# Kernel optimization log

Measured on AMD Instinct MI355X. Metric: run time of the kernel, lower is better.

Reference implementation:

```python
import jax, jax.numpy as jnp
import numpy as np

ALPHA = 0.2          # LeakyReLU negative slope
NEG_INF = -9e15      # mask value from the torch code
B, N, F, E, H, S, T, L = 32, 128, 78, 12, 256, 20, 13, 3


def setup_inputs() -> dict:
    key = jax.random.key(0)
    ks = jax.random.split(key, 20)
    sc = 0.05  # param scale
    inp = {
        "node_features": jax.random.normal(ks[0], (B, N, F), jnp.float32),
        "edge_features": jax.random.normal(ks[1], (B, N, N, E), jnp.float32),
        "adj_matrix": jax.random.randint(ks[2], (B, N, N), 0, 2).astype(jnp.int32),
        "scaffold_features": jax.random.normal(ks[3], (B, S), jnp.float32),
        # node projection (Linear F->H, with bias)
        "W_node": jax.random.normal(ks[4], (F, H), jnp.float32) * sc,
        "b_node": jnp.zeros((H,), jnp.float32),
        # stacked GAT layer params: W (H->H, no bias), a (2H->1, no bias)
        "gat_W": jax.random.normal(ks[5], (L, H, H), jnp.float32) * sc,
        "gat_a": jax.random.normal(ks[6], (L, 2 * H), jnp.float32) * sc,
        # scaffold projection (S->H)
        "W_sc": jax.random.normal(ks[7], (S, H), jnp.float32) * sc,
        "b_sc": jnp.zeros((H,), jnp.float32),
        # graph_pooling MLP: H -> H/2 -> H/4 (shared for graph + scaffold paths)
        "gp_w1": jax.random.normal(ks[8], (H, H // 2), jnp.float32) * sc,
        "gp_b1": jnp.zeros((H // 2,), jnp.float32),
        "gp_w2": jax.random.normal(ks[9], (H // 2, H // 4), jnp.float32) * sc,
        "gp_b2": jnp.zeros((H // 4,), jnp.float32),
        # output MLP: (H/4 + H/4) -> H/2 -> T
        "out_w1": jax.random.normal(ks[10], (H // 2, H // 2), jnp.float32) * sc,
        "out_b1": jnp.zeros((H // 2,), jnp.float32),
        "out_w2": jax.random.normal(ks[11], (H // 2, T), jnp.float32) * sc,
        "out_b2": jnp.zeros((T,), jnp.float32),
    }
    return inp


def _gat_stack(x, adj_matrix, gat_W, gat_a):
    # x: (B,N,H); adj: (B,N,N) int
    mask = adj_matrix > 0
    n_layers, _, h_dim = gat_W.shape
    for l in range(n_layers):
        h = jnp.einsum("bnf,fh->bnh", x, gat_W[l])      # (B,N,H)
        a1, a2 = gat_a[l, :h_dim], gat_a[l, h_dim:]
        # a . [h_i ; h_j] == h_i.a1 + h_j.a2 (exact decomposition of the
        # O(N^2, 2H) concat in the torch code)
        s1 = h @ a1                                       # (B,N)
        s2 = h @ a2                                       # (B,N)
        e = jax.nn.leaky_relu(s1[:, :, None] + s2[:, None, :], ALPHA)
        att = jnp.where(mask, e, NEG_INF)                 # (B,N,N)
        att = jax.nn.softmax(att, axis=-1)
        h_prime = jnp.einsum("bij,bjh->bih", att, h)
        x = jax.nn.relu(h_prime)                          # relu after layer (dropout = identity, eval)
    return x


def _pool(z, gp_w1, gp_b1, gp_w2, gp_b2):
    z = jax.nn.relu(z @ gp_w1 + gp_b1)
    return jax.nn.relu(z @ gp_w2 + gp_b2)


def reference(node_features, edge_features, adj_matrix, scaffold_features,
              W_node, b_node, gat_W, gat_a, W_sc, b_sc,
              gp_w1, gp_b1, gp_w2, gp_b2, out_w1, out_b1, out_w2, out_b2):
    # edge_features is accepted but unused in the original forward
    x = node_features @ W_node + b_node                  # (B,N,H)
    x = _gat_stack(x, adj_matrix, gat_W, gat_a)
    graph = x.mean(axis=1)                               # (B,H)
    g = _pool(graph, gp_w1, gp_b1, gp_w2, gp_b2)         # (B,H/4)
    s = _pool(scaffold_features @ W_sc + b_sc, gp_w1, gp_b1, gp_w2, gp_b2)
    c = jnp.concatenate([g, s], axis=-1)                 # (B,H/2)
    hdn = jax.nn.relu(c @ out_w1 + out_b1)
    return hdn @ out_w2 + out_b2                         # (B,T)
```

## Files before the change

### kernel.cpp

```cpp
#include <hip/hip_runtime.h>
#include <hip/hip_bf16.h>

#define NEG_INF -9.0e15f

using u16 = unsigned short;

__device__ __forceinline__ float b2f(__hip_bfloat16 v) { return __bfloat162float(v); }
__device__ __forceinline__ float ldv(const float* p, int i) { return p[i]; }
__device__ __forceinline__ float ldv(const __hip_bfloat16* p, int i) { return __bfloat162float(p[i]); }
__device__ __forceinline__ float bu2f(u16 u) { return __uint_as_float(((unsigned)u) << 16); }

__device__ __forceinline__ void unpack8u(uint4 r, float* f) {
    f[0]=__uint_as_float(r.x<<16); f[1]=__uint_as_float(r.x&0xffff0000u);
    f[2]=__uint_as_float(r.y<<16); f[3]=__uint_as_float(r.y&0xffff0000u);
    f[4]=__uint_as_float(r.z<<16); f[5]=__uint_as_float(r.z&0xffff0000u);
    f[6]=__uint_as_float(r.w<<16); f[7]=__uint_as_float(r.w&0xffff0000u);
}

__device__ __forceinline__ void async16(const void* g, void* l) {
    __builtin_amdgcn_global_load_lds(
        (__attribute__((address_space(1))) void*)(g),
        (__attribute__((address_space(3))) void*)(l), 16, 0, 0);
}

__device__ __forceinline__ int sniff(const void* wnode) {
    const u16* w = (const u16*)wnode;
    int lane = threadIdx.x & 63;
    u16 u = w[2 * lane];
    int e = (u >> 7) & 0xFF;
    unsigned long long m = __ballot(e >= 100 && e <= 140);
    return __popcll(m) >= 48;
}

__global__ __launch_bounds__(128) void k_gat(
    const float* __restrict__ x, const void* __restrict__ gat_W,
    const void* __restrict__ gat_a, int layer,
    const void* __restrict__ nf, const void* __restrict__ Wn_raw,
    const void* __restrict__ bn, int first,
    float* __restrict__ h, float* __restrict__ s1, float* __restrict__ s2) {
    __shared__ __align__(16) char smem[8192 + 32768 + 2560];
    float* xsT = (float*)smem;
    char*  wb  = smem + 8192;
    float* nfs = (float*)(smem + 8192 + 32768);

    const int t = threadIdx.x, bx = blockIdx.x;
    const int row0 = bx * 8;
    const int rg = t >> 5, cg = t & 31, c0 = 8 * cg;
    const int isbf = sniff(Wn_raw);
    float acc0[8], acc1[8];

    if (isbf) {
        const u16* Wl = (const u16*)gat_W + (size_t)layer * 65536;
        {
            const char* g = (const char*)Wl;
            #pragma unroll
            for (int i = 0; i < 8; ++i)
                async16(g + i * 2048 + t * 16, wb + i * 2048 + t * 16);
        }
        if (first) {
            const u16* nfu = (const u16*)nf;
            for (int i = t; i < 624; i += 128) {
                int r = i / 78, k = i - r * 78;
                nfs[r * 80 + k] = bu2f(nfu[(row0 + r) * 78 + k]);
            }
            __syncthreads();
            const u16* Wnl = (const u16*)Wn_raw;
            float b8[8];
            unpack8u(*(const uint4*)((const u16*)bn + c0), b8);
            #pragma unroll
            for (int j = 0; j < 8; ++j) { acc0[j] = b8[j]; acc1[j] = b8[j]; }
            #pragma unroll 2
            for (int k = 0; k < 78; ++k) {
                float w8[8];
                unpack8u(*(const uint4*)(Wnl + k * 256 + c0), w8);
                float x0 = nfs[(2 * rg) * 80 + k], x1 = nfs[(2 * rg + 1) * 80 + k];
                #pragma unroll
                for (int j = 0; j < 8; ++j) {
                    acc0[j] += x0 * w8[j];
                    acc1[j] += x1 * w8[j];
                }
            }
            #pragma unroll
            for (int j = 0; j < 8; ++j) {
                xsT[(c0 + j) * 8 + 2 * rg]     = acc0[j];
                xsT[(c0 + j) * 8 + 2 * rg + 1] = acc1[j];
            }
            __syncthreads();
        } else {
            int row = t >> 4, kb = (t & 15) * 16;
            const float4* xp = (const float4*)(x + (size_t)(row0 + row) * 256 + kb);
            #pragma unroll
            for (int q = 0; q < 4; ++q) {
                float4 f = xp[q];
                xsT[(kb + 4 * q + 0) * 8 + row] = f.x;
                xsT[(kb + 4 * q + 1) * 8 + row] = f.y;
                xsT[(kb + 4 * q + 2) * 8 + row] = f.z;
                xsT[(kb + 4 * q + 3) * 8 + row] = f.w;
            }
            __syncthreads();
        }
        #pragma unroll
        for (int j = 0; j < 8; ++j) { acc0[j] = 0.f; acc1[j] = 0.f; }
        for (int c = 0; c < 8; ++c) {
            if (c < 7) {
                const char* g = (const char*)Wl + (c + 1) * 16384;
                char* lb = wb + ((c + 1) & 1) * 16384;
                #pragma unroll
                for (int i = 0; i < 8; ++i)
                    async16(g + i * 2048 + t * 16, lb + i * 2048 + t * 16);
            }
            const u16* wc = (const u16*)(wb + (c & 1) * 16384);
            const float* xk = xsT + (c * 32) * 8 + 2 * rg;
            #pragma unroll 4
            for (int kk = 0; kk < 32; ++kk) {
                float w8[8];
                unpack8u(*(const uint4*)(wc + kk * 256 + c0), w8);
                float2 xv = *(const float2*)(xk + kk * 8);
                #pragma unroll
                for (int j = 0; j < 8; ++j) {
                    acc0[j] += xv.x * w8[j];
                    acc1[j] += xv.y * w8[j];
                }
            }
            __syncthreads();
        }
        const u16* ga = (const u16*)gat_a + (size_t)layer * 512;
        float a1v[8], a2v[8];
        unpack8u(*(const uint4*)(ga + c0), a1v);
        unpack8u(*(const uint4*)(ga + 256 + c0), a2v);
        float d10 = 0.f, d20 = 0.f, d11 = 0.f, d21 = 0.f;
        #pragma unroll
        for (int j = 0; j < 8; ++j) {
            d10 += acc0[j] * a1v[j]; d20 += acc0[j] * a2v[j];
            d11 += acc1[j] * a1v[j]; d21 += acc1[j] * a2v[j];
        }
        #pragma unroll
        for (int off = 1; off < 32; off <<= 1) {
            d10 += __shfl_xor(d10, off, 64); d20 += __shfl_xor(d20, off, 64);
            d11 += __shfl_xor(d11, off, 64); d21 += __shfl_xor(d21, off, 64);
        }
        if (cg == 0) {
            s1[row0 + 2 * rg] = d10;     s2[row0 + 2 * rg] = d20;
            s1[row0 + 2 * rg + 1] = d11; s2[row0 + 2 * rg + 1] = d21;
        }
        *(float4*)&h[(size_t)(row0 + 2 * rg) * 256 + c0]         = (float4){acc0[0], acc0[1], acc0[2], acc0[3]};
        *(float4*)&h[(size_t)(row0 + 2 * rg) * 256 + c0 + 4]     = (float4){acc0[4], acc0[5], acc0[6], acc0[7]};
        *(float4*)&h[(size_t)(row0 + 2 * rg + 1) * 256 + c0]     = (float4){acc1[0], acc1[1], acc1[2], acc1[3]};
        *(float4*)&h[(size_t)(row0 + 2 * rg + 1) * 256 + c0 + 4] = (float4){acc1[4], acc1[5], acc1[6], acc1[7]};
    } else {
        float* xs = (float*)smem;
        const float* Wlf = (const float*)gat_W + (size_t)layer * 65536;
        const float* gaf = (const float*)gat_a + (size_t)layer * 512;
        if (first) {
            const float* nff = (const float*)nf;
            for (int i = t; i < 624; i += 128) {
                int r = i / 78, k = i - r * 78;
                nfs[r * 80 + k] = nff[(row0 + r) * 78 + k];
            }
            __syncthreads();
            const float* Wnf = (const float*)Wn_raw;
            const float* bnf = (const float*)bn;
            #pragma unroll
            for (int j = 0; j < 8; ++j) { acc0[j] = bnf[c0 + j]; acc1[j] = acc0[j]; }
            for (int k = 0; k < 78; ++k) {
                float4 w0 = *(const float4*)(Wnf + k * 256 + c0);
                float4 w1 = *(const float4*)(Wnf + k * 256 + c0 + 4);
                float wf[8] = {w0.x, w0.y, w0.z, w0.w, w1.x, w1.y, w1.z, w1.w};
                float x0 = nfs[(2 * rg) * 80 + k], x1 = nfs[(2 * rg + 1) * 80 + k];
                #pragma unroll
                for (int j = 0; j < 8; ++j) { acc0[j] += x0 * wf[j]; acc1[j] += x1 * wf[j]; }
            }
            __syncthreads();
            #pragma unroll
            for (int j = 0; j < 8; ++j) {
                xs[(2 * rg) * 256 + c0 + j]     = acc0[j];
                xs[(2 * rg + 1) * 256 + c0 + j] = acc1[j];
            }
            __syncthreads();
        } else {
            int row = t >> 4, kb = (t & 15) * 16;
            #pragma unroll
            for (int q = 0; q < 4; ++q)
                ((float4*)(xs + row * 256 + kb))[q] =
                    ((const float4*)(x + (size_t)(row0 + row) * 256 + kb))[q];
            __syncthreads();
        }
        #pragma unroll
        for (int j = 0; j < 8; ++j) { acc0[j] = 0.f; acc1[j] = 0.f; }
        #pragma unroll 4
        for (int k = 0; k < 256; ++k) {
            float4 w0 = *(const float4*)(Wlf + k * 256 + c0);
            float4 w1 = *(const float4*)(Wlf + k * 256 + c0 + 4);
            float wf[8] = {w0.x, w0.y, w0.z, w0.w, w1.x, w1.y, w1.z, w1.w};
            float x0 = xs[(2 * rg) * 256 + k], x1 = xs[(2 * rg + 1) * 256 + k];
            #pragma unroll
            for (int j = 0; j < 8; ++j) { acc0[j] += x0 * wf[j]; acc1[j] += x1 * wf[j]; }
        }
        float d10 = 0.f, d20 = 0.f, d11 = 0.f, d21 = 0.f;
        #pragma unroll
        for (int j = 0; j < 8; ++j) {
            float a1v = gaf[c0 + j], a2v = gaf[256 + c0 + j];
            d10 += acc0[j] * a1v; d20 += acc0[j] * a2v;
            d11 += acc1[j] * a1v; d21 += acc1[j] * a2v;
        }
        #pragma unroll
        for (int off = 1; off < 32; off <<= 1) {
            d10 += __shfl_xor(d10, off, 64); d20 += __shfl_xor(d20, off, 64);
            d11 += __shfl_xor(d11, off, 64); d21 += __shfl_xor(d21, off, 64);
        }
        if (cg == 0) {
            s1[row0 + 2 * rg] = d10;     s2[row0 + 2 * rg] = d20;
            s1[row0 + 2 * rg + 1] = d11; s2[row0 + 2 * rg + 1] = d21;
        }
        *(float4*)&h[(size_t)(row0 + 2 * rg) * 256 + c0]         = (float4){acc0[0], acc0[1], acc0[2], acc0[3]};
        *(float4*)&h[(size_t)(row0 + 2 * rg) * 256 + c0 + 4]     = (float4){acc0[4], acc0[5], acc0[6], acc0[7]};
        *(float4*)&h[(size_t)(row0 + 2 * rg + 1) * 256 + c0]     = (float4){acc1[0], acc1[1], acc1[2], acc1[3]};
        *(float4*)&h[(size_t)(row0 + 2 * rg + 1) * 256 + c0 + 4] = (float4){acc1[4], acc1[5], acc1[6], acc1[7]};
    }
}

__global__ __launch_bounds__(256) void k_attn(
    const float* __restrict__ h, const float* __restrict__ s1,
    const float* __restrict__ s2, const int* __restrict__ adj,
    float* __restrict__ x, float* __restrict__ gpart, int do_pool) {
    __shared__ float att_t[128][10];
    __shared__ __align__(16) float hbuf[2][32 * 256];
    __shared__ float pool_red[4][256];
    int blk = blockIdx.x, b = blk >> 4, i0 = (blk & 15) << 3;
    int t = threadIdx.x, w = t >> 6, lane = t & 63;
    const char* hbytes = (const char*)(h + (size_t)b * 32768);
    const int ph = blk & 3;
    {
        char* lb = (char*)&hbuf[0][0];
        const char* g = hbytes + ph * 32768;
        #pragma unroll
        for (int i = 0; i < 8; ++i)
            async16(g + i * 4096 + t * 16, lb + i * 4096 + t * 16);
    }
    {
        int cc0 = lane, cc1 = lane + 64;
        int ir0 = i0 + 2 * w, ir1 = ir0 + 1;
        const int* a0 = adj + (size_t)(b * 128 + ir0) * 128;
        const int* a1 = adj + (size_t)(b * 128 + ir1) * 128;
        int m00 = a0[cc0], m01 = a0[cc1], m10 = a1[cc0], m11 = a1[cc1];
        float sv0 = s1[b * 128 + ir0], sv1 = s1[b * 128 + ir1];
        float t0 = s2[b * 128 + cc0],  t1 = s2[b * 128 + cc1];
        float e00 = sv0 + t0; e00 = (e00 >= 0.f) ? e00 : 0.2f * e00;
        float e01 = sv0 + t1; e01 = (e01 >= 0.f) ? e01 : 0.2f * e01;
        float e10 = sv1 + t0; e10 = (e10 >= 0.f) ? e10 : 0.2f * e10;
        float e11 = sv1 + t1; e11 = (e11 >= 0.f) ? e11 : 0.2f * e11;
        float v00 = (m00 > 0) ? e00 : NEG_INF;
        float v01 = (m01 > 0) ? e01 : NEG_INF;
        float v10 = (m10 > 0) ? e10 : NEG_INF;
        float v11 = (m11 > 0) ? e11 : NEG_INF;
        float mx0 = fmaxf(v00, v01), mx1 = fmaxf(v10, v11);
        #pragma unroll
        for (int off = 1; off < 64; off <<= 1) {
            mx0 = fmaxf(mx0, __shfl_xor(mx0, off, 64));
            mx1 = fmaxf(mx1, __shfl_xor(mx1, off, 64));
        }
        float p00 = __expf(v00 - mx0), p01 = __expf(v01 - mx0);
        float p10 = __expf(v10 - mx1), p11 = __expf(v11 - mx1);
        float s0 = p00 + p01, ss1 = p10 + p11;
        #pragma unroll
        for (int off = 1; off < 64; off <<= 1) {
            s0  += __shfl_xor(s0, off, 64);
            ss1 += __shfl_xor(ss1, off, 64);
        }
        float inv0 = 1.0f / s0, inv1 = 1.0f / ss1;
        att_t[cc0][2 * w]     = p00 * inv0;
        att_t[cc1][2 * w]     = p01 * inv0;
        att_t[cc0][2 * w + 1] = p10 * inv1;
        att_t[cc1][2 * w + 1] = p11 * inv1;
    }
    __syncthreads();
    int tx = t & 63, ty = t >> 6;
    float acc0[4] = {0.f, 0.f, 0.f, 0.f}, acc1[4] = {0.f, 0.f, 0.f, 0.f};
    for (int c = 0; c < 4; ++c) {
        if (c < 3) {
            char* lb = (char*)&hbuf[(c + 1) & 1][0];
            const char* g = hbytes + (((c + 1 + ph) & 3) * 32768);
            #pragma unroll
            for (int i = 0; i < 8; ++i)
                async16(g + i * 4096 + t * 16, lb + i * 4096 + t * 16);
        }
        const float* hc = &hbuf[c & 1][0];
        const int jb = ((c + ph) & 3) * 32;
        #pragma unroll 4
        for (int jj = 0; jj < 32; ++jj) {
            float4 hv = *(const float4*)&hc[jj * 256 + 4 * tx];
            float2 ap = *(const float2*)&att_t[jb + jj][2 * ty];
            acc0[0] += ap.x * hv.x; acc0[1] += ap.x * hv.y;
            acc0[2] += ap.x * hv.z; acc0[3] += ap.x * hv.w;
            acc1[0] += ap.y * hv.x; acc1[1] += ap.y * hv.y;
            acc1[2] += ap.y * hv.z; acc1[3] += ap.y * hv.w;
        }
        __syncthreads();
    }
    if (!do_pool) {
        float4 o0 = {fmaxf(acc0[0],0.f), fmaxf(acc0[1],0.f), fmaxf(acc0[2],0.f), fmaxf(acc0[3],0.f)};
        float4 o1 = {fmaxf(acc1[0],0.f), fmaxf(acc1[1],0.f), fmaxf(acc1[2],0.f), fmaxf(acc1[3],0.f)};
        *(float4*)&x[(size_t)(b * 128 + i0 + 2 * ty)     * 256 + 4 * tx] = o0;
        *(float4*)&x[(size_t)(b * 128 + i0 + 2 * ty + 1) * 256 + 4 * tx] = o1;
    } else {
        float4 pr = {(fmaxf(acc0[0],0.f) + fmaxf(acc1[0],0.f)) * (1.f/128.f),
                     (fmaxf(acc0[1],0.f) + fmaxf(acc1[1],0.f)) * (1.f/128.f),
                     (fmaxf(acc0[2],0.f) + fmaxf(acc1[2],0.f)) * (1.f/128.f),
                     (fmaxf(acc0[3],0.f) + fmaxf(acc1[3],0.f)) * (1.f/128.f)};
        *(float4*)&pool_red[ty][4 * tx] = pr;
        __syncthreads();
        if (t < 64) {
            float4 r0 = ((const float4*)&pool_red[0][0])[t];
            float4 r1 = ((const float4*)&pool_red[1][0])[t];
            float4 r2 = ((const float4*)&pool_red[2][0])[t];
            float4 r3 = ((const float4*)&pool_red[3][0])[t];
            float4 o = {r0.x+r1.x+r2.x+r3.x, r0.y+r1.y+r2.y+r3.y,
                        r0.z+r1.z+r2.z+r3.z, r0.w+r1.w+r2.w+r3.w};
            *(float4*)&gpart[((size_t)b * 16 + (blk & 15)) * 256 + 4 * t] = o;
        }
    }
}

template <typename T>
__device__ __forceinline__ void head_body(
    int b, int t, const float* __restrict__ gpart,
    const T* scaf, const T* W_sc, const T* b_sc,
    const T* gp_w1, const T* gp_b1, const T* gp_w2, const T* gp_b2,
    const T* out_w1, const T* out_b1, const T* out_w2, const T* out_b2,
    float* gin_s, float* sproj, float* scaf_s,
    float* red1, float* red2, float* z1g, float* z1s,
    float* cvec, float* hdn, float* outv) {
    float g = 0.f;
    #pragma unroll
    for (int gg = 0; gg < 16; ++gg) g += gpart[((size_t)b * 16 + gg) * 256 + t];
    gin_s[t] = g;
    if (t < 20) scaf_s[t] = ldv(scaf, b * 20 + t);
    __syncthreads();
    {
        float sa = ldv(b_sc, t);
        #pragma unroll
        for (int k = 0; k < 20; ++k) sa += scaf_s[k] * ldv(W_sc, k * 256 + t);
        sproj[t] = sa;
    }
    __syncthreads();
    {
        int j = t & 127, khalf = t >> 7;
        int k0 = khalf * 128;
        float a1 = 0.f, a2 = 0.f;
        #pragma unroll 16
        for (int kk = 0; kk < 128; ++kk) {
            int k = k0 + kk;
            float wv = ldv(gp_w1, k * 128 + j);
            a1 += gin_s[k] * wv;
            a2 += sproj[k] * wv;
        }
        red1[t] = a1; red2[t] = a2;
    }
    __syncthreads();
    if (t < 128) {
        float bb = ldv(gp_b1, t);
        z1g[t] = fmaxf(bb + red1[t] + red1[t + 128], 0.f);
        z1s[t] = fmaxf(bb + red2[t] + red2[t + 128], 0.f);
    }
    __syncthreads();
    {
        int j = t & 63, q = t >> 6;
        int k0 = q * 32;
        float a1 = 0.f, a2 = 0.f;
        #pragma unroll
        for (int kk = 0; kk < 32; ++kk) {
            int k = k0 + kk;
            float wv = ldv(gp_w2, k * 64 + j);
            a1 += z1g[k] * wv;
            a2 += z1s[k] * wv;
        }
        red1[t] = a1; red2[t] = a2;
    }
    __syncthreads();
    if (t < 64) {
        float bb = ldv(gp_b2, t);
        cvec[t]      = fmaxf(bb + red1[t] + red1[t + 64] + red1[t + 128] + red1[t + 192], 0.f);
        cvec[64 + t] = fmaxf(bb + red2[t] + red2[t + 64] + red2[t + 128] + red2[t + 192], 0.f);
    }
    __syncthreads();
    {
        int j = t & 127, khalf = t >> 7;
        int k0 = khalf * 64;
        float a = 0.f;
        #pragma unroll 16
        for (int kk = 0; kk < 64; ++kk) {
            int k = k0 + kk;
            a += cvec[k] * ldv(out_w1, k * 128 + j);
        }
        red1[t] = a;
    }
    __syncthreads();
    if (t < 128) hdn[t] = fmaxf(ldv(out_b1, t) + red1[t] + red1[t + 128], 0.f);
    __syncthreads();
    if (t < 13) {
        float a = ldv(out_b2, t);
        #pragma unroll 16
        for (int k = 0; k < 128; ++k) a += hdn[k] * ldv(out_w2, k * 13 + t);
        outv[t] = a;
    }
}

__global__ __launch_bounds__(256) void k_head(
    const float* __restrict__ gpart, const void* __restrict__ scaf,
    const void* __restrict__ W_sc, const void* __restrict__ b_sc,
    const void* __restrict__ gp_w1, const void* __restrict__ gp_b1,
    const void* __restrict__ gp_w2, const void* __restrict__ gp_b2,
    const void* __restrict__ out_w1, const void* __restrict__ out_b1,
    const void* __restrict__ out_w2, const void* __restrict__ out_b2,
    void* __restrict__ out, const void* __restrict__ Wn) {
    int isbf = sniff(Wn);
    int b = blockIdx.x;
    int t = threadIdx.x;
    __shared__ float gin_s[256], sproj[256], scaf_s[20];
    __shared__ float red1[256], red2[256];
    __shared__ float z1g[128], z1s[128], cvec[128], hdn[128], outv[13];
    if (isbf) {
        head_body<__hip_bfloat16>(b, t, gpart,
            (const __hip_bfloat16*)scaf, (const __hip_bfloat16*)W_sc, (const __hip_bfloat16*)b_sc,
            (const __hip_bfloat16*)gp_w1, (const __hip_bfloat16*)gp_b1,
            (const __hip_bfloat16*)gp_w2, (const __hip_bfloat16*)gp_b2,
            (const __hip_bfloat16*)out_w1, (const __hip_bfloat16*)out_b1,
            (const __hip_bfloat16*)out_w2, (const __hip_bfloat16*)out_b2,
            gin_s, sproj, scaf_s, red1, red2, z1g, z1s, cvec, hdn, outv);
    } else {
        head_body<float>(b, t, gpart,
            (const float*)scaf, (const float*)W_sc, (const float*)b_sc,
            (const float*)gp_w1, (const float*)gp_b1,
            (const float*)gp_w2, (const float*)gp_b2,
            (const float*)out_w1, (const float*)out_b1,
            (const float*)out_w2, (const float*)out_b2,
            gin_s, sproj, scaf_s, red1, red2, z1g, z1s, cvec, hdn, outv);
    }
    __syncthreads();
    if (t < 13) {
        if (isbf) ((__hip_bfloat16*)out)[b * 13 + t] = __float2bfloat16(outv[t]);
        else      ((float*)out)[b * 13 + t] = outv[t];
    }
}

extern "C" void kernel_launch(void* const* d_in, const int* in_sizes, int n_in,
                              void* d_out, int out_size, void* d_ws, size_t ws_size,
                              hipStream_t stream) {
    (void)in_sizes; (void)n_in; (void)out_size; (void)ws_size;
    const void* nf     = d_in[0];
    const int*  adj    = (const int*)d_in[2];
    const void* scaf   = d_in[3];
    const void* W_node = d_in[4];
    const void* b_node = d_in[5];
    const void* gat_W  = d_in[6];
    const void* gat_a  = d_in[7];
    const void* W_sc   = d_in[8];
    const void* b_sc   = d_in[9];
    const void* gp_w1  = d_in[10];
    const void* gp_b1  = d_in[11];
    const void* gp_w2  = d_in[12];
    const void* gp_b2  = d_in[13];
    const void* out_w1 = d_in[14];
    const void* out_b1 = d_in[15];
    const void* out_w2 = d_in[16];
    const void* out_b2 = d_in[17];

    float* ws    = (float*)d_ws;
    float* x     = ws;
    float* h     = ws + 1048576;
    float* s1    = ws + 2097152;
    float* s2    = s1 + 4096;
    float* gpart = s2 + 4096;

    for (int l = 0; l < 3; ++l) {
        k_gat<<<512, 128, 0, stream>>>(x, gat_W, gat_a, l,
                                       nf, W_node, b_node, (l == 0) ? 1 : 0,
                                       h, s1, s2);
        k_attn<<<512, 256, 0, stream>>>(h, s1, s2, adj, x, gpart, (l == 2) ? 1 : 0);
    }
    k_head<<<32, 256, 0, stream>>>(gpart, scaf, W_sc, b_sc, gp_w1, gp_b1, gp_w2, gp_b2,
                                   out_w1, out_b1, out_w2, out_b2, d_out, W_node);
}
```

Baseline: 229.0 us.

## Fuse attention aggregation with next layer's projection into a single kernel

Adds a kernel that computes the attention softmax and aggregation for one layer, applies ReLU, and immediately multiplies the resulting 8-row tile by the next layer's W to produce h, s1 and s2. This removes the round trip of x through global memory and cuts kernel launches from seven to five. The h tile is staged in smaller chunks with a per-block rotated start offset to spread load across memory. In exchange, each block streams the whole W matrix straight from global memory without LDS staging, and occupancy may drop because shared memory use is higher.

```diff
diff --git a/kernel.cpp b/kernel.cpp
--- a/kernel.cpp
+++ b/kernel.cpp
@@ -33,16 +33,14 @@
 }
 
 __global__ __launch_bounds__(128) void k_gat(
-    const float* __restrict__ x, const void* __restrict__ gat_W,
-    const void* __restrict__ gat_a, int layer,
+    const void* __restrict__ gat_W, const void* __restrict__ gat_a,
     const void* __restrict__ nf, const void* __restrict__ Wn_raw,
-    const void* __restrict__ bn, int first,
+    const void* __restrict__ bn,
     float* __restrict__ h, float* __restrict__ s1, float* __restrict__ s2) {
     __shared__ __align__(16) char smem[8192 + 32768 + 2560];
     float* xsT = (float*)smem;
     char*  wb  = smem + 8192;
     float* nfs = (float*)(smem + 8192 + 32768);
-
     const int t = threadIdx.x, bx = blockIdx.x;
     const int row0 = bx * 8;
     const int rg = t >> 5, cg = t & 31, c0 = 8 * cg;
@@ -50,55 +48,38 @@
     float acc0[8], acc1[8];
 
     if (isbf) {
-        const u16* Wl = (const u16*)gat_W + (size_t)layer * 65536;
+        const u16* Wl = (const u16*)gat_W;
         {
             const char* g = (const char*)Wl;
             #pragma unroll
             for (int i = 0; i < 8; ++i)
                 async16(g + i * 2048 + t * 16, wb + i * 2048 + t * 16);
         }
-        if (first) {
-            const u16* nfu = (const u16*)nf;
-            for (int i = t; i < 624; i += 128) {
-                int r = i / 78, k = i - r * 78;
-                nfs[r * 80 + k] = bu2f(nfu[(row0 + r) * 78 + k]);
-            }
-            __syncthreads();
-            const u16* Wnl = (const u16*)Wn_raw;
-            float b8[8];
-            unpack8u(*(const uint4*)((const u16*)bn + c0), b8);
-            #pragma unroll
-            for (int j = 0; j < 8; ++j) { acc0[j] = b8[j]; acc1[j] = b8[j]; }
-            #pragma unroll 2
-            for (int k = 0; k < 78; ++k) {
-                float w8[8];
-                unpack8u(*(const uint4*)(Wnl + k * 256 + c0), w8);
-                float x0 = nfs[(2 * rg) * 80 + k], x1 = nfs[(2 * rg + 1) * 80 + k];
-                #pragma unroll
-                for (int j = 0; j < 8; ++j) {
-                    acc0[j] += x0 * w8[j];
-                    acc1[j] += x1 * w8[j];
-                }
-            }
-            #pragma unroll
-            for (int j = 0; j < 8; ++j) {
-                xsT[(c0 + j) * 8 + 2 * rg]     = acc0[j];
-                xsT[(c0 + j) * 8 + 2 * rg + 1] = acc1[j];
-            }
-            __syncthreads();
-        } else {
-            int row = t >> 4, kb = (t & 15) * 16;
-            const float4* xp = (const float4*)(x + (size_t)(row0 + row) * 256 + kb);
-            #pragma unroll
-            for (int q = 0; q < 4; ++q) {
-                float4 f = xp[q];
-                xsT[(kb + 4 * q + 0) * 8 + row] = f.x;
-                xsT[(kb + 4 * q + 1) * 8 + row] = f.y;
-                xsT[(kb + 4 * q + 2) * 8 + row] = f.z;
-                xsT[(kb + 4 * q + 3) * 8 + row] = f.w;
-            }
-            __syncthreads();
-        }
+        const u16* nfu = (const u16*)nf;
+        for (int i = t; i < 624; i += 128) {
+            int r = i / 78, k = i - r * 78;
+            nfs[r * 80 + k] = bu2f(nfu[(row0 + r) * 78 + k]);
+        }
+        __syncthreads();
+        const u16* Wnl = (const u16*)Wn_raw;
+        float b8[8];
+        unpack8u(*(const uint4*)((const u16*)bn + c0), b8);
+        #pragma unroll
+        for (int j = 0; j < 8; ++j) { acc0[j] = b8[j]; acc1[j] = b8[j]; }
+        #pragma unroll 2
+        for (int k = 0; k < 78; ++k) {
+            float w8[8];
+            unpack8u(*(const uint4*)(Wnl + k * 256 + c0), w8);
+            float x0 = nfs[(2 * rg) * 80 + k], x1 = nfs[(2 * rg + 1) * 80 + k];
+            #pragma unroll
+            for (int j = 0; j < 8; ++j) { acc0[j] += x0 * w8[j]; acc1[j] += x1 * w8[j]; }
+        }
+        #pragma unroll
+        for (int j = 0; j < 8; ++j) {
+            xsT[(c0 + j) * 8 + 2 * rg]     = acc0[j];
+            xsT[(c0 + j) * 8 + 2 * rg + 1] = acc1[j];
+        }
+        __syncthreads();
         #pragma unroll
         for (int j = 0; j < 8; ++j) { acc0[j] = 0.f; acc1[j] = 0.f; }
         for (int c = 0; c < 8; ++c) {
@@ -117,14 +98,11 @@
                 unpack8u(*(const uint4*)(wc + kk * 256 + c0), w8);
                 float2 xv = *(const float2*)(xk + kk * 8);
                 #pragma unroll
-                for (int j = 0; j < 8; ++j) {
-                    acc0[j] += xv.x * w8[j];
-                    acc1[j] += xv.y * w8[j];
-                }
+                for (int j = 0; j < 8; ++j) { acc0[j] += xv.x * w8[j]; acc1[j] += xv.y * w8[j]; }
             }
             __syncthreads();
         }
-        const u16* ga = (const u16*)gat_a + (size_t)layer * 512;
+        const u16* ga = (const u16*)gat_a;
         float a1v[8], a2v[8];
         unpack8u(*(const uint4*)(ga + c0), a1v);
         unpack8u(*(const uint4*)(ga + 256 + c0), a2v);
@@ -149,42 +127,33 @@
         *(float4*)&h[(size_t)(row0 + 2 * rg + 1) * 256 + c0 + 4] = (float4){acc1[4], acc1[5], acc1[6], acc1[7]};
     } else {
         float* xs = (float*)smem;
-        const float* Wlf = (const float*)gat_W + (size_t)layer * 65536;
-        const float* gaf = (const float*)gat_a + (size_t)layer * 512;
-        if (first) {
-            const float* nff = (const float*)nf;
-            for (int i = t; i < 624; i += 128) {
-                int r = i / 78, k = i - r * 78;
-                nfs[r * 80 + k] = nff[(row0 + r) * 78 + k];
-            }
-            __syncthreads();
-            const float* Wnf = (const float*)Wn_raw;
-            const float* bnf = (const float*)bn;
-            #pragma unroll
-            for (int j = 0; j < 8; ++j) { acc0[j] = bnf[c0 + j]; acc1[j] = acc0[j]; }
-            for (int k = 0; k < 78; ++k) {
-                float4 w0 = *(const float4*)(Wnf + k * 256 + c0);
-                float4 w1 = *(const float4*)(Wnf + k * 256 + c0 + 4);
-                float wf[8] = {w0.x, w0.y, w0.z, w0.w, w1.x, w1.y, w1.z, w1.w};
-                float x0 = nfs[(2 * rg) * 80 + k], x1 = nfs[(2 * rg + 1) * 80 + k];
-                #pragma unroll
-                for (int j = 0; j < 8; ++j) { acc0[j] += x0 * wf[j]; acc1[j] += x1 * wf[j]; }
-            }
-            __syncthreads();
-            #pragma unroll
-            for (int j = 0; j < 8; ++j) {
-                xs[(2 * rg) * 256 + c0 + j]     = acc0[j];
-                xs[(2 * rg + 1) * 256 + c0 + j] = acc1[j];
-            }
-            __syncthreads();
-        } else {
-            int row = t >> 4, kb = (t & 15) * 16;
-            #pragma unroll
-            for (int q = 0; q < 4; ++q)
-                ((float4*)(xs + row * 256 + kb))[q] =
-                    ((const float4*)(x + (size_t)(row0 + row) * 256 + kb))[q];
-            __syncthreads();
-        }
+        const float* Wlf = (const float*)gat_W;
+        const float* gaf = (const float*)gat_a;
+        const float* nff = (const float*)nf;
+        for (int i = t; i < 624; i += 128) {
+            int r = i / 78, k = i - r * 78;
+            nfs[r * 80 + k] = nff[(row0 + r) * 78 + k];
+        }
+        __syncthreads();
+        const float* Wnf = (const float*)Wn_raw;
+        const float* bnf = (const float*)bn;
+        #pragma unroll
+        for (int j = 0; j < 8; ++j) { acc0[j] = bnf[c0 + j]; acc1[j] = acc0[j]; }
+        for (int k = 0; k < 78; ++k) {
+            float4 w0 = *(const float4*)(Wnf + k * 256 + c0);
+            float4 w1 = *(const float4*)(Wnf + k * 256 + c0 + 4);
+            float wf[8] = {w0.x, w0.y, w0.z, w0.w, w1.x, w1.y, w1.z, w1.w};
+            float x0 = nfs[(2 * rg) * 80 + k], x1 = nfs[(2 * rg + 1) * 80 + k];
+            #pragma unroll
+            for (int j = 0; j < 8; ++j) { acc0[j] += x0 * wf[j]; acc1[j] += x1 * wf[j]; }
+        }
+        __syncthreads();
+        #pragma unroll
+        for (int j = 0; j < 8; ++j) {
+            xs[(2 * rg) * 256 + c0 + j]     = acc0[j];
+            xs[(2 * rg + 1) * 256 + c0 + j] = acc1[j];
+        }
+        __syncthreads();
         #pragma unroll
         for (int j = 0; j < 8; ++j) { acc0[j] = 0.f; acc1[j] = 0.f; }
         #pragma unroll 4
@@ -219,10 +188,154 @@
     }
 }
 
+__global__ __launch_bounds__(256) void k_fused(
+    const float* __restrict__ h_in, const float* __restrict__ s1_in,
+    const float* __restrict__ s2_in, const int* __restrict__ adj,
+    const void* __restrict__ gat_W, const void* __restrict__ gat_a, int layer,
+    const void* __restrict__ Wn_raw,
+    float* __restrict__ h_out, float* __restrict__ s1_out, float* __restrict__ s2_out) {
+    __shared__ float att_t[128][10];
+    __shared__ __align__(16) float hbuf[2][16 * 256];
+    __shared__ float xsT[256 * 8];
+    int blk = blockIdx.x, b = blk >> 4, i0 = (blk & 15) << 3;
+    int t = threadIdx.x, w = t >> 6, lane = t & 63;
+    const int isbf = sniff(Wn_raw);
+    const char* hbytes = (const char*)(h_in + (size_t)b * 32768);
+    const int ph = blk & 7;
+    {
+        char* lb = (char*)&hbuf[0][0];
+        const char* g = hbytes + ph * 16384;
+        #pragma unroll
+        for (int i = 0; i < 4; ++i)
+            async16(g + i * 4096 + t * 16, lb + i * 4096 + t * 16);
+    }
+    {
+        int cc0 = lane, cc1 = lane + 64;
+        int ir0 = i0 + 2 * w, ir1 = ir0 + 1;
+        const int* a0 = adj + (size_t)(b * 128 + ir0) * 128;
+        const int* a1 = adj + (size_t)(b * 128 + ir1) * 128;
+        int m00 = a0[cc0], m01 = a0[cc1], m10 = a1[cc0], m11 = a1[cc1];
+        float sv0 = s1_in[b * 128 + ir0], sv1 = s1_in[b * 128 + ir1];
+        float t0 = s2_in[b * 128 + cc0],  t1 = s2_in[b * 128 + cc1];
+        float e00 = sv0 + t0; e00 = (e00 >= 0.f) ? e00 : 0.2f * e00;
+        float e01 = sv0 + t1; e01 = (e01 >= 0.f) ? e01 : 0.2f * e01;
+        float e10 = sv1 + t0; e10 = (e10 >= 0.f) ? e10 : 0.2f * e10;
+        float e11 = sv1 + t1; e11 = (e11 >= 0.f) ? e11 : 0.2f * e11;
+        float v00 = (m00 > 0) ? e00 : NEG_INF;
+        float v01 = (m01 > 0) ? e01 : NEG_INF;
+        float v10 = (m10 > 0) ? e10 : NEG_INF;
+        float v11 = (m11 > 0) ? e11 : NEG_INF;
+        float mx0 = fmaxf(v00, v01), mx1 = fmaxf(v10, v11);
+        #pragma unroll
+        for (int off = 1; off < 64; off <<= 1) {
+            mx0 = fmaxf(mx0, __shfl_xor(mx0, off, 64));
+            mx1 = fmaxf(mx1, __shfl_xor(mx1, off, 64));
+        }
+        float p00 = __expf(v00 - mx0), p01 = __expf(v01 - mx0);
+        float p10 = __expf(v10 - mx1), p11 = __expf(v11 - mx1);
+        float s0 = p00 + p01, ss1 = p10 + p11;
+        #pragma unroll
+        for (int off = 1; off < 64; off <<= 1) {
+            s0  += __shfl_xor(s0, off, 64);
+            ss1 += __shfl_xor(ss1, off, 64);
+        }
+        float inv0 = 1.0f / s0, inv1 = 1.0f / ss1;
+        att_t[cc0][2 * w]     = p00 * inv0;
+        att_t[cc1][2 * w]     = p01 * inv0;
+        att_t[cc0][2 * w + 1] = p10 * inv1;
+        att_t[cc1][2 * w + 1] = p11 * inv1;
+    }
+    __syncthreads();
+    int tx = t & 63, ty = t >> 6;
+    float acc0[4] = {0.f, 0.f, 0.f, 0.f}, acc1[4] = {0.f, 0.f, 0.f, 0.f};
+    for (int c = 0; c < 8; ++c) {
+        if (c < 7) {
+            char* lb = (char*)&hbuf[(c + 1) & 1][0];
+            const char* g = hbytes + (((c + 1 + ph) & 7) * 16384);
+            #pragma unroll
+            for (int i = 0; i < 4; ++i)
+                async16(g + i * 4096 + t * 16, lb + i * 4096 + t * 16);
+        }
+        const float* hc = &hbuf[c & 1][0];
+        const int jb = ((c + ph) & 7) * 16;
+        #pragma unroll 4
+        for (int jj = 0; jj < 16; ++jj) {
+            float4 hv = *(const float4*)&hc[jj * 256 + 4 * tx];
+            float2 ap = *(const float2*)&att_t[jb + jj][2 * ty];
+            acc0[0] += ap.x * hv.x; acc0[1] += ap.x * hv.y;
+            acc0[2] += ap.x * hv.z; acc0[3] += ap.x * hv.w;
+            acc1[0] += ap.y * hv.x; acc1[1] += ap.y * hv.y;
+            acc1[2] += ap.y * hv.z; acc1[3] += ap.y * hv.w;
+        }
+        __syncthreads();
+    }
+    #pragma unroll
+    for (int j = 0; j < 4; ++j) {
+        xsT[(4 * tx + j) * 8 + 2 * ty]     = fmaxf(acc0[j], 0.f);
+        xsT[(4 * tx + j) * 8 + 2 * ty + 1] = fmaxf(acc1[j], 0.f);
+    }
+    __syncthreads();
+    const int r = t >> 5, cg = t & 31, c0 = 8 * cg;
+    const int row0 = blk * 8;
+    float g0[8];
+    #pragma unroll
+    for (int j = 0; j < 8; ++j) g0[j] = 0.f;
+    if (isbf) {
+        const u16* Wl = (const u16*)gat_W + (size_t)layer * 65536;
+        #pragma unroll 4
+        for (int k = 0; k < 256; ++k) {
+            float w8[8];
+            unpack8u(*(const uint4*)(Wl + k * 256 + c0), w8);
+            float xv = xsT[k * 8 + r];
+            #pragma unroll
+            for (int j = 0; j < 8; ++j) g0[j] += xv * w8[j];
+        }
+        const u16* ga = (const u16*)gat_a + (size_t)layer * 512;
+        float a1v[8], a2v[8];
+        unpack8u(*(const uint4*)(ga + c0), a1v);
+        unpack8u(*(const uint4*)(ga + 256 + c0), a2v);
+        float d1 = 0.f, d2 = 0.f;
+        #pragma unroll
+        for (int j = 0; j < 8; ++j) { d1 += g0[j] * a1v[j]; d2 += g0[j] * a2v[j]; }
+        #pragma unroll
+        for (int off = 1; off < 32; off <<= 1) {
+            d1 += __shfl_xor(d1, off, 64);
+            d2 += __shfl_xor(d2, off, 64);
+        }
+        if (cg == 0) { s1_out[row0 + r] = d1; s2_out[row0 + r] = d2; }
+    } else {
+        const float* Wlf = (const float*)gat_W + (size_t)layer * 65536;
+        #pragma unroll 4
+        for (int k = 0; k < 256; ++k) {
+            float4 w0 = *(const float4*)(Wlf + k * 256 + c0);
+            float4 w1 = *(const float4*)(Wlf + k * 256 + c0 + 4);
+            float wf[8] = {w0.x, w0.y, w0.z, w0.w, w1.x, w1.y, w1.z, w1.w};
+            float xv = xsT[k * 8 + r];
+            #pragma unroll
+            for (int j = 0; j < 8; ++j) g0[j] += xv * wf[j];
+        }
+        const float* gaf = (const float*)gat_a + (size_t)layer * 512;
+        float d1 = 0.f, d2 = 0.f;
+        #pragma unroll
+        for (int j = 0; j < 8; ++j) {
+            d1 += g0[j] * gaf[c0 + j];
+            d2 += g0[j] * gaf[256 + c0 + j];
+        }
+        #pragma unroll
+        for (int off = 1; off < 32; off <<= 1) {
+            d1 += __shfl_xor(d1, off, 64);
+            d2 += __shfl_xor(d2, off, 64);
+        }
+        if (cg == 0) { s1_out[row0 + r] = d1; s2_out[row0 + r] = d2; }
+    }
+    *(float4*)&h_out[(size_t)(row0 + r) * 256 + c0]     = (float4){g0[0], g0[1], g0[2], g0[3]};
+    *(float4*)&h_out[(size_t)(row0 + r) * 256 + c0 + 4] = (float4){g0[4], g0[5], g0[6], g0[7]};
+}
+
 __global__ __launch_bounds__(256) void k_attn(
     const float* __restrict__ h, const float* __restrict__ s1,
     const float* __restrict__ s2, const int* __restrict__ adj,
-    float* __restrict__ x, float* __restrict__ gpart, int do_pool) {
+    float* __restrict__ gpart) {
     __shared__ float att_t[128][10];
     __shared__ __align__(16) float hbuf[2][32 * 256];
     __shared__ float pool_red[4][256];
@@ -297,27 +410,20 @@
         }
         __syncthreads();
     }
-    if (!do_pool) {
-        float4 o0 = {fmaxf(acc0[0],0.f), fmaxf(acc0[1],0.f), fmaxf(acc0[2],0.f), fmaxf(acc0[3],0.f)};
-        float4 o1 = {fmaxf(acc1[0],0.f), fmaxf(acc1[1],0.f), fmaxf(acc1[2],0.f), fmaxf(acc1[3],0.f)};
-        *(float4*)&x[(size_t)(b * 128 + i0 + 2 * ty)     * 256 + 4 * tx] = o0;
-        *(float4*)&x[(size_t)(b * 128 + i0 + 2 * ty + 1) * 256 + 4 * tx] = o1;
-    } else {
-        float4 pr = {(fmaxf(acc0[0],0.f) + fmaxf(acc1[0],0.f)) * (1.f/128.f),
-                     (fmaxf(acc0[1],0.f) + fmaxf(acc1[1],0.f)) * (1.f/128.f),
-                     (fmaxf(acc0[2],0.f) + fmaxf(acc1[2],0.f)) * (1.f/128.f),
-                     (fmaxf(acc0[3],0.f) + fmaxf(acc1[3],0.f)) * (1.f/128.f)};
-        *(float4*)&pool_red[ty][4 * tx] = pr;
-        __syncthreads();
-        if (t < 64) {
-            float4 r0 = ((const float4*)&pool_red[0][0])[t];
-            float4 r1 = ((const float4*)&pool_red[1][0])[t];
-            float4 r2 = ((const float4*)&pool_red[2][0])[t];
-            float4 r3 = ((const float4*)&pool_red[3][0])[t];
-            float4 o = {r0.x+r1.x+r2.x+r3.x, r0.y+r1.y+r2.y+r3.y,
-                        r0.z+r1.z+r2.z+r3.z, r0.w+r1.w+r2.w+r3.w};
-            *(float4*)&gpart[((size_t)b * 16 + (blk & 15)) * 256 + 4 * t] = o;
-        }
+    float4 pr = {(fmaxf(acc0[0],0.f) + fmaxf(acc1[0],0.f)) * (1.f/128.f),
+                 (fmaxf(acc0[1],0.f) + fmaxf(acc1[1],0.f)) * (1.f/128.f),
+                 (fmaxf(acc0[2],0.f) + fmaxf(acc1[2],0.f)) * (1.f/128.f),
+                 (fmaxf(acc0[3],0.f) + fmaxf(acc1[3],0.f)) * (1.f/128.f)};
+    *(float4*)&pool_red[ty][4 * tx] = pr;
+    __syncthreads();
+    if (t < 64) {
+        float4 r0 = ((const float4*)&pool_red[0][0])[t];
+        float4 r1 = ((const float4*)&pool_red[1][0])[t];
+        float4 r2 = ((const float4*)&pool_red[2][0])[t];
+        float4 r3 = ((const float4*)&pool_red[3][0])[t];
+        float4 o = {r0.x+r1.x+r2.x+r3.x, r0.y+r1.y+r2.y+r3.y,
+                    r0.z+r1.z+r2.z+r3.z, r0.w+r1.w+r2.w+r3.w};
+        *(float4*)&gpart[((size_t)b * 16 + (blk & 15)) * 256 + 4 * t] = o;
     }
 }
 
@@ -466,18 +572,20 @@
     const void* out_b2 = d_in[17];
 
     float* ws    = (float*)d_ws;
-    float* x     = ws;
-    float* h     = ws + 1048576;
-    float* s1    = ws + 2097152;
-    float* s2    = s1 + 4096;
-    float* gpart = s2 + 4096;
-
-    for (int l = 0; l < 3; ++l) {
-        k_gat<<<512, 128, 0, stream>>>(x, gat_W, gat_a, l,
-                                       nf, W_node, b_node, (l == 0) ? 1 : 0,
-                                       h, s1, s2);
-        k_attn<<<512, 256, 0, stream>>>(h, s1, s2, adj, x, gpart, (l == 2) ? 1 : 0);
-    }
+    float* hA    = ws;
+    float* hB    = ws + 1048576;
+    float* s1A   = ws + 2097152;
+    float* s2A   = s1A + 4096;
+    float* s1B   = s2A + 4096;
+    float* s2B   = s1B + 4096;
+    float* gpart = s2B + 4096;
+
+    k_gat<<<512, 128, 0, stream>>>(gat_W, gat_a, nf, W_node, b_node, hA, s1A, s2A);
+    k_fused<<<512, 256, 0, stream>>>(hA, s1A, s2A, adj, gat_W, gat_a, 1, W_node,
+                                     hB, s1B, s2B);
+    k_fused<<<512, 256, 0, stream>>>(hB, s1B, s2B, adj, gat_W, gat_a, 2, W_node,
+                                     hA, s1A, s2A);
+    k_attn<<<512, 256, 0, stream>>>(hA, s1A, s2A, adj, gpart);
     k_head<<<32, 256, 0, stream>>>(gpart, scaf, W_sc, b_sc, gp_w1, gp_b1, gp_w2, gp_b2,
                                    out_w1, out_b1, out_w2, out_b2, d_out, W_node);
 }
```

Result: no change. 233.1 us (+1.8%).
